# Kernel tuning notes

Measured on AMD Instinct MI355X. Metric: run time of the kernel, lower is better.

The kernel has to match this reference:

```python
import jax, jax.numpy as jnp
import numpy as np

H = 64  # rnn_size == input_size

def setup_inputs() -> dict:
    key = jax.random.key(0)
    ks = jax.random.split(key, 6)
    vocab = 32000
    B, T = 4096, 128
    s = 1.0 / np.sqrt(H)
    return {
        "inst": jax.random.randint(ks[0], (B, T), 0, vocab, dtype=jnp.int64),
        "embed_w": jax.random.normal(ks[1], (vocab + 1, H), dtype=jnp.float32),
        "W_ih": jax.random.uniform(ks[2], (4 * H, H), dtype=jnp.float32, minval=-s, maxval=s),
        "W_hh": jax.random.uniform(ks[3], (4 * H, H), dtype=jnp.float32, minval=-s, maxval=s),
        "b_ih": jax.random.uniform(ks[4], (4 * H,), dtype=jnp.float32, minval=-s, maxval=s),
        "b_hh": jax.random.uniform(ks[5], (4 * H,), dtype=jnp.float32, minval=-s, maxval=s),
    }

def _lstm_scan(xs, W_ih, W_hh, b_ih, b_hh):
    # xs: [T, B, H]. PyTorch LSTMCell gate order: i, f, g, o.
    B = xs.shape[1]
    # Precompute input projections for all timesteps in one big GEMM.
    x_proj = jnp.einsum('tbh,gh->tbg', xs, W_ih) + b_ih + b_hh  # [T, B, 4H]

    def step(carry, xp):
        h, c = carry
        gates = xp + h @ W_hh.T  # [B, 4H]
        i, f, g, o = jnp.split(gates, 4, axis=-1)
        c = jax.nn.sigmoid(f) * c + jax.nn.sigmoid(i) * jnp.tanh(g)
        h = jax.nn.sigmoid(o) * jnp.tanh(c)
        return (h, c), None

    h0 = jnp.zeros((B, H), dtype=xs.dtype)
    c0 = jnp.zeros((B, H), dtype=xs.dtype)
    (h, c), _ = jax.lax.scan(step, (h0, c0), x_proj)
    return h

def reference(inst, embed_w, W_ih, W_hh, b_ih, b_hh):
    # inst: [B, T] int; embedding lookup for whole sequence at once.
    xs = embed_w[inst]                 # [B, T, H]
    xs = jnp.swapaxes(xs, 0, 1)        # [T, B, H] for scan over time
    return _lstm_scan(xs, W_ih, W_hh, b_ih, b_hh)  # final h: [B, H]
```

## Files before the change

kernel.cpp:

```cpp
#include <hip/hip_runtime.h>
#include <hip/hip_bf16.h>

#define H_DIM   64
#define T_STEPS 128
#define B_TOT   4096
#define BB      16
#define SK      72
#define NTHREADS 512
#define XBATCH  8

typedef _Float16 half8  __attribute__((ext_vector_type(8)));
typedef __fp16   fp16x2 __attribute__((ext_vector_type(2)));
typedef __attribute__((ext_vector_type(4))) float f32x4;

#if __has_builtin(__builtin_amdgcn_exp2f)
#define EXP2(x) __builtin_amdgcn_exp2f(x)
#else
#define EXP2(x) exp2f(x)
#endif

__device__ __forceinline__ float sigmoid2(float xp) {
    return __builtin_amdgcn_rcpf(1.0f + EXP2(-xp));
}
__device__ __forceinline__ float tanh2(float xp) {
    return fmaf(-2.0f, __builtin_amdgcn_rcpf(EXP2(xp) + 1.0f), 1.0f);
}

__device__ __forceinline__ float xor8_dpp(float v) {
    return __int_as_float(__builtin_amdgcn_mov_dpp(
        __float_as_int(v), 0x128 , 0xf, 0xf, false));
}

__global__ __launch_bounds__(NTHREADS) void lstm_fused(
    const int* __restrict__ inst, const float* __restrict__ embed,
    const float* __restrict__ Wih, const float* __restrict__ Whh,
    const float* __restrict__ bih, const float* __restrict__ bhh,
    float* __restrict__ out)
{
    __shared__ __align__(16) _Float16 sX[2][BB][SK];
    __shared__ __align__(16) _Float16 sH[2][BB][SK];
    __shared__ int sInst[BB * T_STEPS];

    const int tid  = (int)threadIdx.x;
    const int w    = tid >> 6;
    const int l    = tid & 63;
    const int lrow = l & 15;
    const int lk   = l >> 4;
    const bool losd = (lrow < 8);
    const int c    = w * 8 + (lrow & 7);
    const int b0   = (int)blockIdx.x * BB;

    const float L2E = 1.4426950408889634f;

    for (int i = tid; i < BB * T_STEPS; i += NTHREADS)
        sInst[i] = inst[b0 * T_STEPS + i];

    for (int i = tid; i < BB * SK; i += NTHREADS)
        ((_Float16*)sH)[i] = (_Float16)0.0f;
    __syncthreads();

    half8 wf[2][4];
    float bias[2];
#pragma unroll
    for (int q = 0; q < 2; ++q) {
        const int gate = q * 2 + (lrow >> 3);
        const float wscale = (gate == 2) ? 2.0f * L2E : L2E;
        const int gcol = gate * 64 + c;
        bias[q] = (bih[gcol] + bhh[gcol]) * wscale;
#pragma unroll
        for (int kf = 0; kf < 4; ++kf) {
            const float* src = (kf < 2 ? Wih : Whh) + (long)gcol * H_DIM + (kf & 1) * 32 + lk * 8;
            half8 v;
#pragma unroll
            for (int j = 0; j < 8; ++j) v[j] = (_Float16)(src[j] * wscale);
            wf[q][kf] = v;
        }
    }

    const int xr = tid >> 5;
    const int xc = tid & 31;
    {
        const int idx = sInst[xr * T_STEPS + 0];
        const float2 xv = *reinterpret_cast<const float2*>(embed + (long)idx * H_DIM + xc * 2);
        fp16x2 hp = __builtin_amdgcn_cvt_pkrtz(xv.x, xv.y);
        *reinterpret_cast<fp16x2*>(&sX[0][xr][xc * 2]) = hp;
    }

    float2 xbuf[XBATCH];
#pragma unroll
    for (int j = 0; j < XBATCH; ++j) {
        const int idx = sInst[xr * T_STEPS + 1 + j];
        xbuf[j] = *reinterpret_cast<const float2*>(embed + (long)idx * H_DIM + xc * 2);
    }
    __syncthreads();

    float creg[2] = {0.f, 0.f};
    float hreg[2] = {0.f, 0.f};

    for (int tb = 0; tb < T_STEPS; tb += XBATCH) {
#pragma unroll
        for (int j = 0; j < XBATCH; ++j) {
            const int t   = tb + j;
            const int buf = j & 1;
            const int ob  = buf ^ 1;
            const bool pf = (t + 1 < T_STEPS);

            const float2 xcur = xbuf[j];

            if (j == XBATCH - 1 && pf) {
#pragma unroll
                for (int jj = 0; jj < XBATCH; ++jj) {
                    const int tt = t + 2 + jj;
                    if (tt < T_STEPS) {
                        const int idx = sInst[xr * T_STEPS + tt];
                        xbuf[jj] = *reinterpret_cast<const float2*>(embed + (long)idx * H_DIM + xc * 2);
                    }
                }
            }

            half8 a0 = *reinterpret_cast<const half8*>(&sX[buf][lrow][lk * 8]);
            half8 a1 = *reinterpret_cast<const half8*>(&sX[buf][lrow][32 + lk * 8]);
            half8 a2 = *reinterpret_cast<const half8*>(&sH[buf][lrow][lk * 8]);
            half8 a3 = *reinterpret_cast<const half8*>(&sH[buf][lrow][32 + lk * 8]);

            f32x4 acc[2];
#pragma unroll
            for (int q = 0; q < 2; ++q) {
                f32x4 pA = {bias[q], bias[q], bias[q], bias[q]};
                f32x4 pB = {0.f, 0.f, 0.f, 0.f};
                pA = __builtin_amdgcn_mfma_f32_16x16x32_f16(a0, wf[q][0], pA, 0, 0, 0);
                pB = __builtin_amdgcn_mfma_f32_16x16x32_f16(a1, wf[q][1], pB, 0, 0, 0);
                pA = __builtin_amdgcn_mfma_f32_16x16x32_f16(a2, wf[q][2], pA, 0, 0, 0);
                pB = __builtin_amdgcn_mfma_f32_16x16x32_f16(a3, wf[q][3], pB, 0, 0, 0);
                acc[q] = pA + pB;
            }

            const float e0 = xor8_dpp(losd ? acc[0][2] : acc[0][0]);
            const float e1 = xor8_dpp(losd ? acc[0][3] : acc[0][1]);
            const float e2 = xor8_dpp(losd ? acc[1][2] : acc[1][0]);
            const float e3 = xor8_dpp(losd ? acc[1][3] : acc[1][1]);

#pragma unroll
            for (int jr = 0; jr < 2; ++jr) {
                const int r  = (losd ? 0 : 2) + jr;
                const float ea = jr ? e1 : e0;
                const float eb = jr ? e3 : e2;
                const float vi = losd ? acc[0][r] : ea;
                const float vf = losd ? ea        : acc[0][r];
                const float vg = losd ? acc[1][r] : eb;
                const float vo = losd ? eb        : acc[1][r];
                const float iv = sigmoid2(vi);
                const float fv = sigmoid2(vf);
                const float gv = tanh2(vg);
                const float ov = sigmoid2(vo);
                const float cn = fv * creg[jr] + iv * gv;
                creg[jr] = cn;
                hreg[jr] = ov * tanh2(cn * (2.0f * L2E));

                if (pf) {
                    const int row = lk * 4 + r;
                    sH[ob][row][c] = (_Float16)hreg[jr];
                }
            }

            if (pf) {
                fp16x2 hp = __builtin_amdgcn_cvt_pkrtz(xcur.x, xcur.y);
                *reinterpret_cast<fp16x2*>(&sX[ob][xr][xc * 2]) = hp;
            }
            __syncthreads();
        }
    }

#pragma unroll
    for (int j = 0; j < 2; ++j) {
        const int row = lk * 4 + (losd ? 0 : 2) + j;
        out[(long)(b0 + row) * H_DIM + c] = hreg[j];
    }
}

extern "C" void kernel_launch(void* const* d_in, const int* in_sizes, int n_in,
                              void* d_out, int out_size, void* d_ws, size_t ws_size,
                              hipStream_t stream) {
    const int*   inst  = (const int*)  d_in[0];
    const float* embed = (const float*)d_in[1];
    const float* Wih   = (const float*)d_in[2];
    const float* Whh   = (const float*)d_in[3];
    const float* bih   = (const float*)d_in[4];
    const float* bhh   = (const float*)d_in[5];
    float* out = (float*)d_out;

    lstm_fused<<<B_TOT / BB, NTHREADS, 0, stream>>>(inst, embed, Wih, Whh, bih, bhh, out);
}
```

Baseline: 93.37 us.

## Halve batch per block to 8 rows, doubling grid and columns per wave

```diff
diff --git a/kernel.cpp b/kernel.cpp
--- a/kernel.cpp
+++ b/kernel.cpp
@@ -4,9 +4,9 @@
 #define H_DIM   64
 #define T_STEPS 128
 #define B_TOT   4096
-#define BB      16
+#define BB      8
 #define SK      72
-#define NTHREADS 512
+#define NTHREADS 256
 #define XBATCH  8
 
 typedef _Float16 half8  __attribute__((ext_vector_type(8)));
@@ -37,8 +37,8 @@
     const float* __restrict__ bih, const float* __restrict__ bhh,
     float* __restrict__ out)
 {
-    __shared__ __align__(16) _Float16 sX[2][BB][SK];
-    __shared__ __align__(16) _Float16 sH[2][BB][SK];
+    __shared__ __align__(16) _Float16 sX[2][16][SK];
+    __shared__ __align__(16) _Float16 sH[2][16][SK];
     __shared__ int sInst[BB * T_STEPS];
 
     const int tid  = (int)threadIdx.x;
@@ -47,43 +47,53 @@
     const int lrow = l & 15;
     const int lk   = l >> 4;
     const bool losd = (lrow < 8);
-    const int c    = w * 8 + (lrow & 7);
-    const int b0   = (int)blockIdx.x * BB;
+    const int colbase = w * 16 + (lrow & 7);
+    const int rstar = losd ? 0 : 1;
+    const int mrow  = lk * 4 + rstar;
+    const int br    = lk * 2 + rstar;
+    const int b0    = (int)blockIdx.x * BB;
 
-    const float L2E = 1.4426950408889634f;
+    const float L2E     = 1.4426950408889634f;
+    const float TWO_L2E = 2.8853900817779268f;
 
     for (int i = tid; i < BB * T_STEPS; i += NTHREADS)
         sInst[i] = inst[b0 * T_STEPS + i];
 
-    for (int i = tid; i < BB * SK; i += NTHREADS)
+    for (int i = tid; i < 2 * 16 * SK; i += NTHREADS) {
+        ((_Float16*)sX)[i] = (_Float16)0.0f;
         ((_Float16*)sH)[i] = (_Float16)0.0f;
+    }
     __syncthreads();
 
-    half8 wf[2][4];
-    float bias[2];
+    half8 wf[2][2][4];
+    float bias[2][2];
 #pragma unroll
-    for (int q = 0; q < 2; ++q) {
-        const int gate = q * 2 + (lrow >> 3);
-        const float wscale = (gate == 2) ? 2.0f * L2E : L2E;
-        const int gcol = gate * 64 + c;
-        bias[q] = (bih[gcol] + bhh[gcol]) * wscale;
+    for (int cg = 0; cg < 2; ++cg) {
 #pragma unroll
-        for (int kf = 0; kf < 4; ++kf) {
-            const float* src = (kf < 2 ? Wih : Whh) + (long)gcol * H_DIM + (kf & 1) * 32 + lk * 8;
-            half8 v;
+        for (int q = 0; q < 2; ++q) {
+            const int gate = q * 2 + (lrow >> 3);
+            const float ws = (gate == 2) ? TWO_L2E : L2E;
+            const int gcol = gate * 64 + colbase + cg * 8;
+            bias[cg][q] = (bih[gcol] + bhh[gcol]) * ws;
 #pragma unroll
-            for (int j = 0; j < 8; ++j) v[j] = (_Float16)(src[j] * wscale);
-            wf[q][kf] = v;
+            for (int kf = 0; kf < 4; ++kf) {
+                const float* src = (kf < 2 ? Wih : Whh) + (long)gcol * H_DIM + (kf & 1) * 32 + lk * 8;
+                half8 v;
+#pragma unroll
+                for (int jj = 0; jj < 8; ++jj) v[jj] = (_Float16)(src[jj] * ws);
+                wf[cg][q][kf] = v;
+            }
         }
     }
 
     const int xr = tid >> 5;
     const int xc = tid & 31;
+    const int xm = (xr >> 1) * 4 + (xr & 1);
     {
         const int idx = sInst[xr * T_STEPS + 0];
         const float2 xv = *reinterpret_cast<const float2*>(embed + (long)idx * H_DIM + xc * 2);
         fp16x2 hp = __builtin_amdgcn_cvt_pkrtz(xv.x, xv.y);
-        *reinterpret_cast<fp16x2*>(&sX[0][xr][xc * 2]) = hp;
+        *reinterpret_cast<fp16x2*>(&sX[0][xm][xc * 2]) = hp;
     }
 
     float2 xbuf[XBATCH];
@@ -123,59 +133,54 @@
             half8 a2 = *reinterpret_cast<const half8*>(&sH[buf][lrow][lk * 8]);
             half8 a3 = *reinterpret_cast<const half8*>(&sH[buf][lrow][32 + lk * 8]);
 
-            f32x4 acc[2];
+            f32x4 acc[2][2];
 #pragma unroll
-            for (int q = 0; q < 2; ++q) {
-                f32x4 pA = {bias[q], bias[q], bias[q], bias[q]};
-                f32x4 pB = {0.f, 0.f, 0.f, 0.f};
-                pA = __builtin_amdgcn_mfma_f32_16x16x32_f16(a0, wf[q][0], pA, 0, 0, 0);
-                pB = __builtin_amdgcn_mfma_f32_16x16x32_f16(a1, wf[q][1], pB, 0, 0, 0);
-                pA = __builtin_amdgcn_mfma_f32_16x16x32_f16(a2, wf[q][2], pA, 0, 0, 0);
-                pB = __builtin_amdgcn_mfma_f32_16x16x32_f16(a3, wf[q][3], pB, 0, 0, 0);
-                acc[q] = pA + pB;
+            for (int cg = 0; cg < 2; ++cg) {
+#pragma unroll
+                for (int q = 0; q < 2; ++q) {
+                    f32x4 a = {bias[cg][q], bias[cg][q], bias[cg][q], bias[cg][q]};
+                    a = __builtin_amdgcn_mfma_f32_16x16x32_f16(a0, wf[cg][q][0], a, 0, 0, 0);
+                    a = __builtin_amdgcn_mfma_f32_16x16x32_f16(a1, wf[cg][q][1], a, 0, 0, 0);
+                    a = __builtin_amdgcn_mfma_f32_16x16x32_f16(a2, wf[cg][q][2], a, 0, 0, 0);
+                    a = __builtin_amdgcn_mfma_f32_16x16x32_f16(a3, wf[cg][q][3], a, 0, 0, 0);
+                    acc[cg][q] = a;
+                }
             }
 
-            const float e0 = xor8_dpp(losd ? acc[0][2] : acc[0][0]);
-            const float e1 = xor8_dpp(losd ? acc[0][3] : acc[0][1]);
-            const float e2 = xor8_dpp(losd ? acc[1][2] : acc[1][0]);
-            const float e3 = xor8_dpp(losd ? acc[1][3] : acc[1][1]);
+#pragma unroll
+            for (int cg = 0; cg < 2; ++cg) {
+                const float loc0 = losd ? acc[cg][0][0] : acc[cg][0][1];
+                const float loc1 = losd ? acc[cg][1][0] : acc[cg][1][1];
+                const float rem0 = xor8_dpp(losd ? acc[cg][0][1] : acc[cg][0][0]);
+                const float rem1 = xor8_dpp(losd ? acc[cg][1][1] : acc[cg][1][0]);
+                const float vi = losd ? loc0 : rem0;
+                const float vf = losd ? rem0 : loc0;
+                const float vg = losd ? loc1 : rem1;
+                const float vo = losd ? rem1 : loc1;
 
-#pragma unroll
-            for (int jr = 0; jr < 2; ++jr) {
-                const int r  = (losd ? 0 : 2) + jr;
-                const float ea = jr ? e1 : e0;
-                const float eb = jr ? e3 : e2;
-                const float vi = losd ? acc[0][r] : ea;
-                const float vf = losd ? ea        : acc[0][r];
-                const float vg = losd ? acc[1][r] : eb;
-                const float vo = losd ? eb        : acc[1][r];
                 const float iv = sigmoid2(vi);
                 const float fv = sigmoid2(vf);
                 const float gv = tanh2(vg);
                 const float ov = sigmoid2(vo);
-                const float cn = fv * creg[jr] + iv * gv;
-                creg[jr] = cn;
-                hreg[jr] = ov * tanh2(cn * (2.0f * L2E));
+                const float g2 = gv * TWO_L2E;
+                const float cs = fmaf(fv, creg[cg], iv * g2);
+                creg[cg] = cs;
+                hreg[cg] = ov * tanh2(cs);
 
-                if (pf) {
-                    const int row = lk * 4 + r;
-                    sH[ob][row][c] = (_Float16)hreg[jr];
-                }
+                if (pf)
+                    sH[ob][mrow][colbase + cg * 8] = (_Float16)hreg[cg];
             }
 
             if (pf) {
                 fp16x2 hp = __builtin_amdgcn_cvt_pkrtz(xcur.x, xcur.y);
-                *reinterpret_cast<fp16x2*>(&sX[ob][xr][xc * 2]) = hp;
+                *reinterpret_cast<fp16x2*>(&sX[ob][xm][xc * 2]) = hp;
             }
             __syncthreads();
         }
     }
 
-#pragma unroll
-    for (int j = 0; j < 2; ++j) {
-        const int row = lk * 4 + (losd ? 0 : 2) + j;
-        out[(long)(b0 + row) * H_DIM + c] = hreg[j];
-    }
+    out[(long)(b0 + br) * H_DIM + colbase]     = hreg[0];
+    out[(long)(b0 + br) * H_DIM + colbase + 8] = hreg[1];
 }
 
 extern "C" void kernel_launch(void* const* d_in, const int* in_sizes, int n_in,
```

Result: slower. 99.53 us (+6.6%).
